# Kernel tuning notes

Hardware: AMD Instinct MI355X
Metric: run time of the kernel (lower is better)

The kernel has to match this reference:

```python
import jax, jax.numpy as jnp
import numpy as np

D = 1024
H = 16
HD = D // H
FF = 4 * D
EPS = 1e-5


def _ln(x, alpha, shift):
    mean = jnp.mean(x, axis=-1, keepdims=True)
    var = jnp.mean(jnp.square(x - mean), axis=-1, keepdims=True)  # biased var
    return alpha * (x - mean) / jnp.sqrt(var + EPS) + shift


def _gelu(x):
    c = jnp.sqrt(jnp.asarray(2.0 / jnp.pi, x.dtype))
    return 0.5 * x * (1.0 + jnp.tanh(c * (x + 0.044715 * x * x * x)))


def setup_inputs() -> dict:
    key = jax.random.key(0)
    ks = jax.random.split(key, 8)
    B, T = 2, 2048
    s_d = 1.0 / np.sqrt(D)
    s_f = 1.0 / np.sqrt(FF)
    return {
        "x": jax.random.normal(ks[0], (B, T, D), jnp.float32),
        "wq": jax.random.normal(ks[1], (D, D), jnp.float32) * s_d,
        "wk": jax.random.normal(ks[2], (D, D), jnp.float32) * s_d,
        "wv": jax.random.normal(ks[3], (D, D), jnp.float32) * s_d,
        "wo": jax.random.normal(ks[4], (D, D), jnp.float32) * s_d,
        "bo": jnp.zeros((D,), jnp.float32),
        "w1": jax.random.normal(ks[5], (D, FF), jnp.float32) * s_d,
        "b1": jnp.zeros((FF,), jnp.float32),
        "w2": jax.random.normal(ks[6], (FF, D), jnp.float32) * s_f,
        "b2": jnp.zeros((D,), jnp.float32),
        "a1": jnp.ones((D,), jnp.float32),
        "s1": jnp.zeros((D,), jnp.float32),
        "a2": jnp.ones((D,), jnp.float32),
        "s2": jnp.zeros((D,), jnp.float32),
    }


def reference(x, wq, wk, wv, wo, bo, w1, b1, w2, b2, a1, s1, a2, s2):
    B, T, _ = x.shape
    # --- pre-LN + causal MHA ---
    h = _ln(x, a1, s1)
    q = (h @ wq).reshape(B, T, H, HD).transpose(0, 2, 1, 3)  # [B,H,T,hd]
    k = (h @ wk).reshape(B, T, H, HD).transpose(0, 2, 1, 3)
    v = (h @ wv).reshape(B, T, H, HD).transpose(0, 2, 1, 3)
    scores = jnp.einsum('bhqd,bhkd->bhqk', q, k) / np.sqrt(HD)
    causal = jnp.tril(jnp.ones((T, T), bool))
    scores = jnp.where(causal, scores, -jnp.inf)
    weights = jax.nn.softmax(scores, axis=-1)
    ctx = jnp.einsum('bhqk,bhkd->bhqd', weights, v)
    ctx = ctx.transpose(0, 2, 1, 3).reshape(B, T, D)
    x = x + (ctx @ wo + bo)
    # --- pre-LN + GELU FFN ---
    h = _ln(x, a2, s2)
    h = _gelu(h @ w1 + b1) @ w2 + b2
    return x + h
```

## Files before the change

### kernel.cpp

```cpp
#include <hip/hip_runtime.h>
#include <hip/hip_bf16.h>

typedef __bf16 bf16x8 __attribute__((ext_vector_type(8)));
typedef float floatx4 __attribute__((ext_vector_type(4)));

constexpr int Dm = 1024;
constexpr int Hh = 16;
constexpr int HD = 64;
constexpr int FF = 4096;
constexpr int Tt = 2048;
constexpr int Bb = 2;
constexpr int MR = Bb * Tt;

typedef const __attribute__((address_space(1))) void* gas1p;
typedef __attribute__((address_space(3))) void* las3p;

__global__ __launch_bounds__(256) void transpose_bf16_kernel(
    const float* __restrict__ W, __hip_bfloat16* __restrict__ WT, int K, int N) {
  __shared__ float tile[32][33];
  int n0 = blockIdx.x * 32, k0 = blockIdx.y * 32;
  int tx = threadIdx.x, ty = threadIdx.y;
#pragma unroll
  for (int i = 0; i < 4; ++i) {
    int k = k0 + ty + i * 8;
    tile[ty + i * 8][tx] = W[(size_t)k * N + n0 + tx];
  }
  __syncthreads();
#pragma unroll
  for (int i = 0; i < 4; ++i) {
    int n = n0 + ty + i * 8;
    WT[(size_t)n * K + k0 + tx] = __float2bfloat16(tile[tx][ty + i * 8]);
  }
}

__global__ __launch_bounds__(256) void ln_bf16_kernel(
    const float* __restrict__ x, const float* __restrict__ alpha,
    const float* __restrict__ shift, __hip_bfloat16* __restrict__ out) {
  int row = blockIdx.x;
  const float4 v = ((const float4*)(x + (size_t)row * Dm))[threadIdx.x];
  float s = v.x + v.y + v.z + v.w;
  float ss = v.x * v.x + v.y * v.y + v.z * v.z + v.w * v.w;
#pragma unroll
  for (int o = 32; o; o >>= 1) {
    s += __shfl_down(s, o);
    ss += __shfl_down(ss, o);
  }
  __shared__ float rs[4], rss[4];
  int w = threadIdx.x >> 6, lane = threadIdx.x & 63;
  if (lane == 0) { rs[w] = s; rss[w] = ss; }
  __syncthreads();
  float tot = rs[0] + rs[1] + rs[2] + rs[3];
  float tots = rss[0] + rss[1] + rss[2] + rss[3];
  float mean = tot * (1.f / Dm);
  float var = tots * (1.f / Dm) - mean * mean;
  float rstd = rsqrtf(var + 1e-5f);
  int col = threadIdx.x * 4;
  __hip_bfloat16* op = out + (size_t)row * Dm + col;
  float vv[4] = {v.x, v.y, v.z, v.w};
#pragma unroll
  for (int e = 0; e < 4; ++e)
    op[e] = __float2bfloat16((vv[e] - mean) * rstd * alpha[col + e] + shift[col + e]);
}

template <int EPI, int TM>
__global__ __launch_bounds__(256) void gemm_tiled(
    const __bf16* __restrict__ A, const __bf16* __restrict__ BT,
    void* __restrict__ Cout, const float* __restrict__ bias,
    const float* __restrict__ resid, int M, int N, int K) {
  constexpr int ANL = TM / 64;
  constexpr int NI = (TM == 128) ? 4 : 2;
  constexpr int WN = (TM == 128) ? 64 : 32;
  __shared__ __bf16 As[3][TM * 32];
  __shared__ __bf16 Bs[3][128 * 32];
  const int tid = threadIdx.x;
  const int w = tid >> 6, lane = tid & 63;
  const int r16 = lane & 15, quad = lane >> 4;
  const int wm = (TM == 128) ? (w & 1) : 0;
  const int wn = (TM == 128) ? (w >> 1) : w;
  const int m0 = blockIdx.y * TM;
  const int n0 = blockIdx.x * 128;

  int sa_row[ANL], sa_gcb[ANL];
#pragma unroll
  for (int p = 0; p < ANL; ++p) {
    int idx = tid + p * 256;
    sa_row[p] = idx >> 2;
    sa_gcb[p] = (idx & 3) ^ ((sa_row[p] >> 1) & 3);
  }
  int sb_row[2], sb_gcb[2];
#pragma unroll
  for (int p = 0; p < 2; ++p) {
    int idx = tid + p * 256;
    sb_row[p] = idx >> 2;
    sb_gcb[p] = (idx & 3) ^ ((sb_row[p] >> 1) & 3);
  }

  int aoffL[4], boffL[NI];
#pragma unroll
  for (int i = 0; i < 4; ++i) {
    int ra = wm * 64 + i * 16 + r16;
    aoffL[i] = ra * 32 + (quad ^ ((ra >> 1) & 3)) * 8;
  }
#pragma unroll
  for (int i = 0; i < NI; ++i) {
    int rb = wn * WN + i * 16 + r16;
    boffL[i] = rb * 32 + (quad ^ ((rb >> 1) & 3)) * 8;
  }

  auto stage = [&](int kt, int buf) {
    int k0 = kt * 32;
#pragma unroll
    for (int p = 0; p < ANL; ++p)
      __builtin_amdgcn_global_load_lds(
          (gas1p)(A + (size_t)(m0 + sa_row[p]) * K + k0 + sa_gcb[p] * 8),
          (las3p)(&As[buf][(tid + p * 256) * 8]), 16, 0, 0);
#pragma unroll
    for (int p = 0; p < 2; ++p)
      __builtin_amdgcn_global_load_lds(
          (gas1p)(BT + (size_t)(n0 + sb_row[p]) * K + k0 + sb_gcb[p] * 8),
          (las3p)(&Bs[buf][(tid + p * 256) * 8]), 16, 0, 0);
  };

  floatx4 acc[4][NI] = {};
  const int nk = K / 32;
  stage(0, 0);
  stage(1, 1);
  for (int kt = 0; kt < nk; ++kt) {
    int cur = kt - (kt / 3) * 3;
    if (kt + 1 < nk) {
      if constexpr (ANL == 2)
        asm volatile("s_waitcnt vmcnt(4) lgkmcnt(0)\n\ts_barrier" ::: "memory");
      else
        asm volatile("s_waitcnt vmcnt(3) lgkmcnt(0)\n\ts_barrier" ::: "memory");
    } else {
      asm volatile("s_waitcnt vmcnt(0) lgkmcnt(0)\n\ts_barrier" ::: "memory");
    }
    if (kt + 2 < nk) {
      int nb = kt + 2;
      nb -= (nb / 3) * 3;
      stage(kt + 2, nb);
    }
    bf16x8 a[4], b[NI];
#pragma unroll
    for (int i = 0; i < 4; ++i) a[i] = *reinterpret_cast<const bf16x8*>(&As[cur][aoffL[i]]);
#pragma unroll
    for (int i = 0; i < NI; ++i) b[i] = *reinterpret_cast<const bf16x8*>(&Bs[cur][boffL[i]]);
#pragma unroll
    for (int mi = 0; mi < 4; ++mi)
#pragma unroll
      for (int ni = 0; ni < NI; ++ni)
        acc[mi][ni] = __builtin_amdgcn_mfma_f32_16x16x32_bf16(a[mi], b[ni], acc[mi][ni], 0, 0, 0);
  }

#pragma unroll
  for (int mi = 0; mi < 4; ++mi)
#pragma unroll
    for (int ni = 0; ni < NI; ++ni)
#pragma unroll
      for (int r = 0; r < 4; ++r) {
        int row = m0 + wm * 64 + mi * 16 + quad * 4 + r;
        int col = n0 + wn * WN + ni * 16 + r16;
        float vacc = acc[mi][ni][r];
        if (EPI == 1) {
          vacc += bias[col] + resid[(size_t)row * N + col];
          ((float*)Cout)[(size_t)row * N + col] = vacc;
        } else if (EPI == 2) {
          vacc += bias[col];
          float u = vacc + 0.044715f * vacc * vacc * vacc;
          float e = __builtin_amdgcn_exp2f(2.3025851f * u);
          float th = 1.f - 2.f * __builtin_amdgcn_rcpf(e + 1.f);
          ((__hip_bfloat16*)Cout)[(size_t)row * N + col] =
              __float2bfloat16(0.5f * vacc * (1.f + th));
        } else {
          int bb = row >> 11, t = row & 2047;
          int qkv = col >> 10, rem = col & 1023;
          int h = rem >> 6, d = rem & 63;
          ((__hip_bfloat16*)Cout)[(size_t)qkv * (MR * Dm) +
                                  ((size_t)(bb * Hh + h) * Tt + t) * HD + d] =
              __float2bfloat16(vacc);
        }
      }
}

__global__ __launch_bounds__(256) void vtrans_kernel(
    const __bf16* __restrict__ vin, __bf16* __restrict__ vout) {
  __shared__ __bf16 tile[64][72];
  int bh = blockIdx.x, t0 = blockIdx.y * 64;
  int tid = threadIdx.x;
#pragma unroll
  for (int p = 0; p < 2; ++p) {
    int idx = tid + p * 256;
    int r = idx >> 3, c = (idx & 7) * 8;
    *reinterpret_cast<bf16x8*>(&tile[r][c]) =
        *reinterpret_cast<const bf16x8*>(vin + ((size_t)bh * Tt + t0 + r) * HD + c);
  }
  __syncthreads();
#pragma unroll
  for (int p = 0; p < 2; ++p) {
    int idx = tid + p * 256;
    int d = idx >> 3, c = (idx & 7) * 8;
    bf16x8 v;
#pragma unroll
    for (int j = 0; j < 8; ++j) v[j] = tile[c + j][d];
    *reinterpret_cast<bf16x8*>(vout + ((size_t)bh * HD + d) * Tt + t0 + c) = v;
  }
}

__global__ __launch_bounds__(256) void attn_kernel(
    const __bf16* __restrict__ qp, const __bf16* __restrict__ kp,
    const __bf16* __restrict__ vtp, __bf16* __restrict__ ctx) {
  __shared__ __bf16 Ks[2][64 * 64];
  __shared__ __bf16 Vt[2][80 * 64];
  __shared__ __bf16 Ps[4 * 16 * 72];
  int bh = blockIdx.x;
  int b = bh >> 4, h = bh & 15;
  int qt = 31 - blockIdx.y;
  int tid = threadIdx.x;
  int w = tid >> 6, lane = tid & 63;
  int r16 = lane & 15, quad = lane >> 4;
  int q0 = qt * 64;
  const size_t base = (size_t)bh * Tt * HD;

  {
    int r = 64 + (tid >> 4);
    int c = (tid & 15) * 4;
    __bf16 val = (r == 64) ? (__bf16)1.0f : (__bf16)0.0f;
#pragma unroll
    for (int bu = 0; bu < 2; ++bu) {
      __bf16* p = &Vt[bu][r * 64 + c];
      p[0] = val; p[1] = val; p[2] = val; p[3] = val;
    }
  }

  const float QS = 0.125f * 1.44269504088896f;
  bf16x8 aq[2];
#pragma unroll
  for (int ks = 0; ks < 2; ++ks) {
    bf16x8 t = *reinterpret_cast<const bf16x8*>(
        qp + base + (size_t)(q0 + w * 16 + r16) * HD + ks * 32 + quad * 8);
#pragma unroll
    for (int j = 0; j < 8; ++j) t[j] = (__bf16)((float)t[j] * QS);
    aq[ks] = t;
  }

  auto stage = [&](int kt, int buf) {
#pragma unroll
    for (int p = 0; p < 2; ++p) {
      int idx = tid + p * 256;
      int row = idx >> 3, c = idx & 7;
      int gc = c ^ (row & 7);
      __builtin_amdgcn_global_load_lds(
          (gas1p)(kp + base + (size_t)(kt * 64 + row) * HD + gc * 8),
          (las3p)(&Ks[buf][idx * 8]), 16, 0, 0);
      __builtin_amdgcn_global_load_lds(
          (gas1p)(vtp + base + (size_t)row * Tt + kt * 64 + gc * 8),
          (las3p)(&Vt[buf][idx * 8]), 16, 0, 0);
    }
  };

  floatx4 O[5] = {};
  stage(0, 0);
  for (int kt = 0; kt <= qt; ++kt) {
    int cur = kt & 1;
    __syncthreads();
    if (kt < qt) stage(kt + 1, cur ^ 1);

    floatx4 sacc[4] = {};
#pragma unroll
    for (int ks = 0; ks < 2; ++ks)
#pragma unroll
      for (int ni = 0; ni < 4; ++ni) {
        int row = ni * 16 + r16;
        bf16x8 bk = *reinterpret_cast<const bf16x8*>(
            &Ks[cur][row * 64 + (((ks << 2) | quad) ^ (r16 & 7)) * 8]);
        sacc[ni] = __builtin_amdgcn_mfma_f32_16x16x32_bf16(aq[ks], bk, sacc[ni], 0, 0, 0);
      }

    bool diag = (kt == qt);
#pragma unroll
    for (int ni = 0; ni < 4; ++ni)
#pragma unroll
      for (int r = 0; r < 4; ++r) {
        float sv = sacc[ni][r];
        if (diag)
          sv = (ni * 16 + r16 <= w * 16 + quad * 4 + r) ? sv : -__builtin_inff();
        Ps[w * 1152 + (quad * 4 + r) * 72 + ni * 16 + r16] =
            (__bf16)__builtin_amdgcn_exp2f(sv);
      }

#pragma unroll
    for (int ks = 0; ks < 2; ++ks) {
      bf16x8 ap = *reinterpret_cast<const bf16x8*>(
          &Ps[w * 1152 + r16 * 72 + ks * 32 + quad * 8]);
#pragma unroll
      for (int ni = 0; ni < 5; ++ni) {
        int row = ni * 16 + r16;
        bf16x8 bv = *reinterpret_cast<const bf16x8*>(
            &Vt[cur][row * 64 + (((ks << 2) | quad) ^ (r16 & 7)) * 8]);
        O[ni] = __builtin_amdgcn_mfma_f32_16x16x32_bf16(ap, bv, O[ni], 0, 0, 0);
      }
    }
  }

  float invl[4];
#pragma unroll
  for (int r = 0; r < 4; ++r) {
    float l = __shfl(O[4][r], lane & 48);
    invl[r] = 1.f / l;
  }
#pragma unroll
  for (int r = 0; r < 4; ++r) {
    int qrow = q0 + w * 16 + quad * 4 + r;
    __bf16* op = ctx + ((size_t)(b * Tt + qrow)) * Dm + h * HD;
#pragma unroll
    for (int ni = 0; ni < 4; ++ni)
      op[ni * 16 + r16] = (__bf16)(O[ni][r] * invl[r]);
  }
}

extern "C" void kernel_launch(void* const* d_in, const int* in_sizes, int n_in,
                              void* d_out, int out_size, void* d_ws, size_t ws_size,
                              hipStream_t stream) {
  const float* x = (const float*)d_in[0];
  const float* wq = (const float*)d_in[1];
  const float* wk = (const float*)d_in[2];
  const float* wv = (const float*)d_in[3];
  const float* wo = (const float*)d_in[4];
  const float* bo = (const float*)d_in[5];
  const float* w1 = (const float*)d_in[6];
  const float* b1 = (const float*)d_in[7];
  const float* w2 = (const float*)d_in[8];
  const float* b2 = (const float*)d_in[9];
  const float* a1 = (const float*)d_in[10];
  const float* s1 = (const float*)d_in[11];
  const float* a2 = (const float*)d_in[12];
  const float* s2 = (const float*)d_in[13];
  float* out = (float*)d_out;
  char* ws = (char*)d_ws;

  const size_t MB = 1024 * 1024;
  __hip_bfloat16* WqkvT = (__hip_bfloat16*)(ws + 0 * MB);
  __hip_bfloat16* WkT = (__hip_bfloat16*)(ws + 2 * MB);
  __hip_bfloat16* WvT = (__hip_bfloat16*)(ws + 4 * MB);
  __hip_bfloat16* WoT = (__hip_bfloat16*)(ws + 6 * MB);
  __hip_bfloat16* W1T = (__hip_bfloat16*)(ws + 8 * MB);
  __hip_bfloat16* W2T = (__hip_bfloat16*)(ws + 16 * MB);
  __hip_bfloat16* h1  = (__hip_bfloat16*)(ws + 24 * MB);
  __hip_bfloat16* qkvb = (__hip_bfloat16*)(ws + 32 * MB);
  __hip_bfloat16* ctxb = (__hip_bfloat16*)(ws + 56 * MB);
  __hip_bfloat16* h2  = (__hip_bfloat16*)(ws + 64 * MB);
  __hip_bfloat16* g   = (__hip_bfloat16*)(ws + 72 * MB);
  __hip_bfloat16* vtb = (__hip_bfloat16*)(ws + 104 * MB);

  dim3 tb(32, 8);
  transpose_bf16_kernel<<<dim3(Dm / 32, Dm / 32), tb, 0, stream>>>(wq, WqkvT, Dm, Dm);
  transpose_bf16_kernel<<<dim3(Dm / 32, Dm / 32), tb, 0, stream>>>(wk, WkT, Dm, Dm);
  transpose_bf16_kernel<<<dim3(Dm / 32, Dm / 32), tb, 0, stream>>>(wv, WvT, Dm, Dm);
  transpose_bf16_kernel<<<dim3(Dm / 32, Dm / 32), tb, 0, stream>>>(wo, WoT, Dm, Dm);
  transpose_bf16_kernel<<<dim3(FF / 32, Dm / 32), tb, 0, stream>>>(w1, W1T, Dm, FF);
  transpose_bf16_kernel<<<dim3(Dm / 32, FF / 32), tb, 0, stream>>>(w2, W2T, FF, Dm);

  ln_bf16_kernel<<<MR, 256, 0, stream>>>(x, a1, s1, h1);

  gemm_tiled<3, 128><<<dim3(3 * Dm / 128, MR / 128), 256, 0, stream>>>(
      (const __bf16*)h1, (const __bf16*)WqkvT, qkvb, nullptr, nullptr, MR, 3 * Dm, Dm);

  vtrans_kernel<<<dim3(Bb * Hh, Tt / 64), 256, 0, stream>>>(
      (const __bf16*)(qkvb + 2 * (size_t)MR * Dm), (__bf16*)vtb);

  attn_kernel<<<dim3(Bb * Hh, Tt / 64), 256, 0, stream>>>(
      (const __bf16*)qkvb, (const __bf16*)(qkvb + (size_t)MR * Dm),
      (const __bf16*)vtb, (__bf16*)ctxb);

  gemm_tiled<1, 64><<<dim3(Dm / 128, MR / 64), 256, 0, stream>>>(
      (const __bf16*)ctxb, (const __bf16*)WoT, out, bo, x, MR, Dm, Dm);

  ln_bf16_kernel<<<MR, 256, 0, stream>>>(out, a2, s2, h2);

  gemm_tiled<2, 128><<<dim3(FF / 128, MR / 128), 256, 0, stream>>>(
      (const __bf16*)h2, (const __bf16*)W1T, g, b1, nullptr, MR, FF, Dm);

  gemm_tiled<1, 64><<<dim3(Dm / 128, MR / 64), 256, 0, stream>>>(
      (const __bf16*)g, (const __bf16*)W2T, out, b2, out, MR, Dm, FF);
}
```

Before: 374.2 us.

## Load GEMM B operand straight to registers and use a four-stage LDS ring for A

The B tile no longer goes through shared memory. Each wave loads its B fragments directly from global memory into a four-deep register ring, while A keeps a four-buffer LDS ring. The main loop is unrolled by four with explicit vmcnt waits sized to cover both kinds of in-flight loads. The aim is to remove B's LDS write and read traffic and shrink LDS use. In exchange, B is fetched redundantly per wave through L2 in less coalesced 16-byte row pieces, and the extra B buffers add register pressure.

```diff
diff --git a/kernel.cpp b/kernel.cpp
--- a/kernel.cpp
+++ b/kernel.cpp
@@ -70,8 +70,7 @@
   constexpr int ANL = TM / 64;
   constexpr int NI = (TM == 128) ? 4 : 2;
   constexpr int WN = (TM == 128) ? 64 : 32;
-  __shared__ __bf16 As[3][TM * 32];
-  __shared__ __bf16 Bs[3][128 * 32];
+  __shared__ __bf16 As[4 * TM * 32];
   const int tid = threadIdx.x;
   const int w = tid >> 6, lane = tid & 63;
   const int r16 = lane & 15, quad = lane >> 4;
@@ -87,69 +86,77 @@
     sa_row[p] = idx >> 2;
     sa_gcb[p] = (idx & 3) ^ ((sa_row[p] >> 1) & 3);
   }
-  int sb_row[2], sb_gcb[2];
-#pragma unroll
-  for (int p = 0; p < 2; ++p) {
-    int idx = tid + p * 256;
-    sb_row[p] = idx >> 2;
-    sb_gcb[p] = (idx & 3) ^ ((sb_row[p] >> 1) & 3);
-  }
-
-  int aoffL[4], boffL[NI];
+
+  int aoffL[4];
 #pragma unroll
   for (int i = 0; i < 4; ++i) {
     int ra = wm * 64 + i * 16 + r16;
     aoffL[i] = ra * 32 + (quad ^ ((ra >> 1) & 3)) * 8;
   }
-#pragma unroll
-  for (int i = 0; i < NI; ++i) {
-    int rb = wn * WN + i * 16 + r16;
-    boffL[i] = rb * 32 + (quad ^ ((rb >> 1) & 3)) * 8;
-  }
-
-  auto stage = [&](int kt, int buf) {
+
+  const __bf16* bp[NI];
+#pragma unroll
+  for (int i = 0; i < NI; ++i)
+    bp[i] = BT + (size_t)(n0 + wn * WN + i * 16 + r16) * K + quad * 8;
+
+  bf16x8 breg[4][NI];
+  floatx4 acc[4][NI] = {};
+
+  auto stageA = [&](int kt, int buf) {
     int k0 = kt * 32;
 #pragma unroll
     for (int p = 0; p < ANL; ++p)
       __builtin_amdgcn_global_load_lds(
           (gas1p)(A + (size_t)(m0 + sa_row[p]) * K + k0 + sa_gcb[p] * 8),
-          (las3p)(&As[buf][(tid + p * 256) * 8]), 16, 0, 0);
-#pragma unroll
-    for (int p = 0; p < 2; ++p)
-      __builtin_amdgcn_global_load_lds(
-          (gas1p)(BT + (size_t)(n0 + sb_row[p]) * K + k0 + sb_gcb[p] * 8),
-          (las3p)(&Bs[buf][(tid + p * 256) * 8]), 16, 0, 0);
-  };
-
-  floatx4 acc[4][NI] = {};
+          (las3p)(&As[buf * TM * 32 + (tid + p * 256) * 8]), 16, 0, 0);
+  };
+  auto loadB = [&](int kt, bf16x8 (&dst)[NI]) {
+#pragma unroll
+    for (int i = 0; i < NI; ++i)
+      dst[i] = *reinterpret_cast<const bf16x8*>(bp[i] + kt * 32);
+  };
+  auto wait2 = [&]() {
+    if constexpr (TM == 128)
+      asm volatile("s_waitcnt vmcnt(12) lgkmcnt(0)\n\ts_barrier" ::: "memory");
+    else
+      asm volatile("s_waitcnt vmcnt(6) lgkmcnt(0)\n\ts_barrier" ::: "memory");
+  };
+  auto wait1 = [&]() {
+    if constexpr (TM == 128)
+      asm volatile("s_waitcnt vmcnt(6) lgkmcnt(0)\n\ts_barrier" ::: "memory");
+    else
+      asm volatile("s_waitcnt vmcnt(3) lgkmcnt(0)\n\ts_barrier" ::: "memory");
+  };
+  auto wait0 = [&]() {
+    asm volatile("s_waitcnt vmcnt(0) lgkmcnt(0)\n\ts_barrier" ::: "memory");
+  };
+  auto compute = [&](int buf, bf16x8 (&bc)[NI]) {
+    bf16x8 a[4];
+#pragma unroll
+    for (int i = 0; i < 4; ++i)
+      a[i] = *reinterpret_cast<const bf16x8*>(&As[buf * TM * 32 + aoffL[i]]);
+#pragma unroll
+    for (int mi = 0; mi < 4; ++mi)
+#pragma unroll
+      for (int ni = 0; ni < NI; ++ni)
+        acc[mi][ni] = __builtin_amdgcn_mfma_f32_16x16x32_bf16(a[mi], bc[ni], acc[mi][ni], 0, 0, 0);
+  };
+
   const int nk = K / 32;
-  stage(0, 0);
-  stage(1, 1);
-  for (int kt = 0; kt < nk; ++kt) {
-    int cur = kt - (kt / 3) * 3;
-    if (kt + 1 < nk) {
-      if constexpr (ANL == 2)
-        asm volatile("s_waitcnt vmcnt(4) lgkmcnt(0)\n\ts_barrier" ::: "memory");
-      else
-        asm volatile("s_waitcnt vmcnt(3) lgkmcnt(0)\n\ts_barrier" ::: "memory");
-    } else {
-      asm volatile("s_waitcnt vmcnt(0) lgkmcnt(0)\n\ts_barrier" ::: "memory");
-    }
-    if (kt + 2 < nk) {
-      int nb = kt + 2;
-      nb -= (nb / 3) * 3;
-      stage(kt + 2, nb);
-    }
-    bf16x8 a[4], b[NI];
-#pragma unroll
-    for (int i = 0; i < 4; ++i) a[i] = *reinterpret_cast<const bf16x8*>(&As[cur][aoffL[i]]);
-#pragma unroll
-    for (int i = 0; i < NI; ++i) b[i] = *reinterpret_cast<const bf16x8*>(&Bs[cur][boffL[i]]);
-#pragma unroll
-    for (int mi = 0; mi < 4; ++mi)
-#pragma unroll
-      for (int ni = 0; ni < NI; ++ni)
-        acc[mi][ni] = __builtin_amdgcn_mfma_f32_16x16x32_bf16(a[mi], b[ni], acc[mi][ni], 0, 0, 0);
+  stageA(0, 0); loadB(0, breg[0]);
+  stageA(1, 1); loadB(1, breg[1]);
+  for (int kt = 0; kt + 4 < nk; kt += 4) {
+    stageA(kt + 2, 2); loadB(kt + 2, breg[2]); wait2(); compute(0, breg[0]);
+    stageA(kt + 3, 3); loadB(kt + 3, breg[3]); wait2(); compute(1, breg[1]);
+    stageA(kt + 4, 0); loadB(kt + 4, breg[0]); wait2(); compute(2, breg[2]);
+    stageA(kt + 5, 1); loadB(kt + 5, breg[1]); wait2(); compute(3, breg[3]);
+  }
+  {
+    int kt = nk - 4;
+    stageA(kt + 2, 2); loadB(kt + 2, breg[2]); wait2(); compute(0, breg[0]);
+    stageA(kt + 3, 3); loadB(kt + 3, breg[3]); wait2(); compute(1, breg[1]);
+    wait1(); compute(2, breg[2]);
+    wait0(); compute(3, breg[3]);
   }
 
 #pragma unroll
```

Measured after the change: 426.8 us. +14.0%, slower.
